# Kernel tuning notes

Hardware: AMD Instinct MI355X
Metric: run time of the kernel (lower is better)

## Reference

```python
import jax, jax.numpy as jnp
import numpy as np

B, N, DIM, H, CH, M = 2, 65536, 256, 8, 32, 64
INNER = H * CH  # 256


def setup_inputs() -> dict:
    key = jax.random.key(0)
    ks = jax.random.split(key, 13)
    s = 0.02
    return {
        "x": jax.random.normal(ks[0], (B, N, DIM), dtype=jnp.float32),
        "W_fx": jax.random.normal(ks[1], (DIM, INNER), dtype=jnp.float32) * s,
        "b_fx": jnp.zeros((INNER,), dtype=jnp.float32),
        "W_x": jax.random.normal(ks[2], (DIM, INNER), dtype=jnp.float32) * s,
        "b_x": jnp.zeros((INNER,), dtype=jnp.float32),
        "W_slice": jax.random.normal(ks[3], (CH, M), dtype=jnp.float32) * s,
        "b_slice": jnp.zeros((M,), dtype=jnp.float32),
        "temperature": 0.5 * jnp.ones((1, H, 1, 1), dtype=jnp.float32),
        "W_q": jax.random.normal(ks[4], (CH, CH), dtype=jnp.float32) * s,
        "W_k": jax.random.normal(ks[5], (CH, CH), dtype=jnp.float32) * s,
        "W_v": jax.random.normal(ks[6], (CH, CH), dtype=jnp.float32) * s,
        "W_out": jax.random.normal(ks[7], (INNER, DIM), dtype=jnp.float32) * s,
        "b_out": jnp.zeros((DIM,), dtype=jnp.float32),
    }


def reference(x, W_fx, b_fx, W_x, b_x, W_slice, b_slice, temperature,
              W_q, W_k, W_v, W_out, b_out):
    b, n, _ = x.shape
    h, ch, m = H, CH, M
    # input projections -> [B, H, N, Ch]
    fx_mid = (x @ W_fx + b_fx).reshape(b, n, h, ch).transpose(0, 2, 1, 3)
    x_mid = (x @ W_x + b_x).reshape(b, n, h, ch).transpose(0, 2, 1, 3)
    # learned soft-slice weights: [B, H, N, M]
    temp = jnp.clip(temperature, 0.1, 5.0)
    logits = (x_mid @ W_slice + b_slice) / temp
    slice_weights = jax.nn.softmax(logits, axis=-1)
    slice_norm = slice_weights.sum(axis=2)  # [B, H, M]
    # aggregate N points into M slice tokens: [B, H, M, Ch]
    slice_token = jnp.einsum('bhnc,bhng->bhgc', fx_mid, slice_weights)
    slice_token = slice_token / (slice_norm + 1e-5)[:, :, :, None]
    # small attention among slice tokens
    q = slice_token @ W_q
    k = slice_token @ W_k
    v = slice_token @ W_v
    scale = ch ** (-0.5)
    attn = jax.nn.softmax(jnp.einsum('bhgc,bhkc->bhgk', q, k) * scale, axis=-1)
    out_slice = attn @ v  # [B, H, M, Ch]
    # scatter back to N points: [B, H, N, Ch] -> [B, N, H*Ch]
    out_x = jnp.einsum('bhgc,bhng->bhnc', out_slice, slice_weights)
    out_x = out_x.transpose(0, 2, 1, 3).reshape(b, n, h * ch)
    return out_x @ W_out + b_out
```

## Files before the change

kernel.cpp:

```cpp
#include <hip/hip_runtime.h>

#define N_ 65536

typedef unsigned int  uint32;
typedef unsigned short ushort;
typedef float  f32x4 __attribute__((ext_vector_type(4)));
typedef short  s16x8 __attribute__((ext_vector_type(8)));
typedef uint32 u32x2 __attribute__((ext_vector_type(2)));
typedef uint32 u32x4 __attribute__((ext_vector_type(4)));

__device__ __forceinline__ uint32 f2bf(float f){
  union{float f; uint32 i;} v; v.f=f;
  return (v.i + 0x7fffu + ((v.i>>16)&1u)) >> 16;
}
__device__ __forceinline__ float bfl(uint32 h){
  union{uint32 i; float f;} v; v.i = h<<16; return v.f;
}
__device__ __forceinline__ uint32 pk2(float a, float b){
  return f2bf(a) | (f2bf(b)<<16);
}
__device__ __forceinline__ f32x4 mfma16(s16x8 a, s16x8 b, f32x4 c){
  return __builtin_amdgcn_mfma_f32_16x16x32_bf16(a,b,c,0,0,0);
}
__device__ __forceinline__ s16x8 mk8(uint32 a, uint32 b, uint32 c, uint32 d){
  union{u32x4 u; s16x8 s;} v; v.u = (u32x4){a,b,c,d}; return v.s;
}

__global__ __launch_bounds__(256) void prep_kernel(
    const float* __restrict__ Wfx, const float* __restrict__ Wx,
    const float* __restrict__ Wsl, const float* __restrict__ bsl,
    const float* __restrict__ bx,  const float* __restrict__ temp,
    ushort* __restrict__ WlT, ushort* __restrict__ WfxT, float* __restrict__ blT)
{
  const int blk = blockIdx.x, t = threadIdx.x;
  if (blk < 512){
    const int m = blk, h = m>>6, mp = m&63;
    const float tmp = fminf(fmaxf(temp[h],0.1f),5.0f);
    float s = 0.f;
    #pragma unroll
    for (int cc=0; cc<32; cc++) s += Wx[t*256 + h*32+cc]*Wsl[cc*64+mp];
    WlT[m*256+t] = (ushort)f2bf(s/tmp);
    if (t==0){
      float bs = bsl[mp];
      for (int cc=0; cc<32; cc++) bs += bx[h*32+cc]*Wsl[cc*64+mp];
      blT[m] = bs/tmp;
    }
  } else {
    const int c = blk-512;
    WfxT[c*256+t] = (ushort)f2bf(Wfx[t*256+c]);
  }
}

__global__ __launch_bounds__(256) void xbf_kernel(const float* __restrict__ x, ushort* __restrict__ xbf)
{
  const size_t i = ((size_t)blockIdx.x*256 + threadIdx.x)*8;
  const float4* xp = (const float4*)(x + i);
  const float4 a = xp[0], b = xp[1];
  u32x4 o; o.x = pk2(a.x,a.y); o.y = pk2(a.z,a.w); o.z = pk2(b.x,b.y); o.w = pk2(b.z,b.w);
  *(u32x4*)(xbf + i) = o;
}

__global__ __launch_bounds__(512)
void k1a_kernel(
    const ushort* __restrict__ xbf,
    const ushort* __restrict__ WlT,
    const ushort* __restrict__ WfxT,
    const float* __restrict__ blT,
    const float* __restrict__ bfx,
    ushort* __restrict__ swg2,
    float* __restrict__ stp,
    float* __restrict__ normp)
{
  __shared__ __align__(16) char smem[98304];
  const int t = threadIdx.x;
  const int w = t>>6, l = t&63, rg = l>>4, c16 = l&15;
  const int blk = blockIdx.x;
  const int tile0 = ((blk&127)<<3) + ((blk>>7)<<10);

  char* swb = smem + 65536 + (w<<12);

  f32x4 pc[2][4];
  #pragma unroll
  for (int i=0;i<2;i++)
    #pragma unroll
    for (int j=0;j<4;j++) pc[i][j] = (f32x4){0.f,0.f,0.f,0.f};
  f32x4 nacc[4];
  #pragma unroll
  for (int i=0;i<4;i++) nacc[i] = (f32x4){0.f,0.f,0.f,0.f};
  float bfv[2];
  #pragma unroll
  for (int cf=0;cf<2;cf++) bfv[cf] = bfx[(w<<5)+(cf<<4)+c16];

  #define STAGE(TILE, BUF) { \
    const int gnS = (int)((TILE)<<6); \
    _Pragma("unroll") \
    for (int p=0;p<4;p++){ \
      const int row = (p<<4) + (t>>5); \
      const int z = (t&31)<<4; \
      const char* g = (const char*)xbf + (((size_t)(gnS+row))<<9) + (size_t)(z ^ ((row&7)<<4)); \
      uint32* ldsp = (uint32*)(smem + ((BUF)<<15) + (p<<13) + ((t>>6)<<10)); \
      __builtin_amdgcn_global_load_lds((const uint32*)g, ldsp, 16, 0, 0); \
    } }

  STAGE(tile0, 0);
  __syncthreads();

  for (int it=0; it<8; ++it){
    const int cur = it&1;
    const int tile = tile0 + it;
    if (it<7) STAGE(tile+1, cur^1);
    const char* Xb = smem + (cur<<15);
    const long gn0 = (long)tile<<6;

    #pragma unroll
    for (int ch=0; ch<2; ch++){
      f32x4 accA[4][2];
      #pragma unroll
      for (int mf=0;mf<4;mf++)
        #pragma unroll
        for (int nfc=0;nfc<2;nfc++) accA[mf][nfc] = (f32x4){0.f,0.f,0.f,0.f};
      #pragma unroll
      for (int kb=0;kb<8;kb++){
        s16x8 aW[4], xv[2];
        #pragma unroll
        for (int mf=0;mf<4;mf++)
          aW[mf] = *(const s16x8*)(WlT + (((w<<6)+(mf<<4)+c16)<<8) + (kb<<5)+(rg<<3));
        #pragma unroll
        for (int nfc=0;nfc<2;nfc++){
          const int row = (ch<<5) + (nfc<<4) + c16;
          xv[nfc] = *(const s16x8*)(Xb + (row<<9) + (((kb<<6)+(rg<<4)) ^ ((row&7)<<4)));
        }
        #pragma unroll
        for (int mf=0;mf<4;mf++)
          #pragma unroll
          for (int nfc=0;nfc<2;nfc++)
            accA[mf][nfc] = mfma16(aW[mf], xv[nfc], accA[mf][nfc]);
      }
      #pragma unroll
      for (int nfc=0;nfc<2;nfc++){
        f32x4 v[4];
        float mx = -3.0e38f;
        #pragma unroll
        for (int mf=0;mf<4;mf++){
          const f32x4 bl4 = *(const f32x4*)(blT + (w<<6)+(mf<<4)+(rg<<2));
          v[mf] = accA[mf][nfc] + bl4;
          mx = fmaxf(mx, fmaxf(fmaxf(v[mf].x, v[mf].y), fmaxf(v[mf].z, v[mf].w)));
        }
        mx = fmaxf(mx, __shfl_xor(mx,16));
        mx = fmaxf(mx, __shfl_xor(mx,32));
        float s = 0.f;
        #pragma unroll
        for (int mf=0;mf<4;mf++){
          v[mf].x = __expf(v[mf].x-mx); v[mf].y = __expf(v[mf].y-mx);
          v[mf].z = __expf(v[mf].z-mx); v[mf].w = __expf(v[mf].w-mx);
          s += v[mf].x+v[mf].y+v[mf].z+v[mf].w;
        }
        s += __shfl_xor(s,16);
        s += __shfl_xor(s,32);
        const float inv = 1.0f/s;
        const int pb = (int)(gn0>>4) + (ch<<1) + nfc;
        #pragma unroll
        for (int mf=0;mf<4;mf++){
          f32x4 sv = v[mf]*inv;
          nacc[mf] += sv;
          u32x2 p; p.x = pk2(sv.x, sv.y); p.y = pk2(sv.z, sv.w);
          *(u32x2*)(swg2 + ((((((size_t)pb<<3)+w)<<2)+mf)<<8) + (rg<<6) + (c16<<2)) = p;
          const uint32 px = (uint32)__shfl_xor((int)p.x, 1);
          const uint32 py = (uint32)__shfl_xor((int)p.y, 1);
          const bool ev = ((c16&1)==0);
          const uint32 s0 = ev ? (uint32)p.x : py;
          const uint32 s1 = ev ? px : (uint32)p.y;
          const uint32 wA = (s0 & 0xffffu) | (s1<<16);
          const uint32 wB = (s0>>16) | (s1 & 0xffff0000u);
          const int rowA = (mf<<4) + (rg<<2) + (ev?0:2);
          const int cbyt = ((nfc<<4) | (c16 & ~1)) << 1;
          *(uint32*)(swb + ((rowA  )<<6) + (cbyt ^ (((rowA  )&7)<<3))) = wA;
          *(uint32*)(swb + ((rowA+1)<<6) + (cbyt ^ (((rowA+1)&7)<<3))) = wB;
        }
      }

      f32x4 accB[2][2];
      #pragma unroll
      for (int pf=0;pf<2;pf++)
        #pragma unroll
        for (int cf=0;cf<2;cf++) accB[pf][cf] = (f32x4){0.f,0.f,0.f,0.f};
      #pragma unroll
      for (int kb=0;kb<8;kb++){
        s16x8 bW[2], xv[2];
        #pragma unroll
        for (int cf=0;cf<2;cf++)
          bW[cf] = *(const s16x8*)(WfxT + (((w<<5)+(cf<<4)+c16)<<8) + (kb<<5)+(rg<<3));
        #pragma unroll
        for (int pf=0;pf<2;pf++){
          const int row = (ch<<5) + (pf<<4) + c16;
          xv[pf] = *(const s16x8*)(Xb + (row<<9) + (((kb<<6)+(rg<<4)) ^ ((row&7)<<4)));
        }
        #pragma unroll
        for (int pf=0;pf<2;pf++)
          #pragma unroll
          for (int cf=0;cf<2;cf++)
            accB[pf][cf] = mfma16(xv[pf], bW[cf], accB[pf][cf]);
      }
      u32x4 afu[2][2];
      #pragma unroll
      for (int cf=0;cf<2;cf++)
        #pragma unroll
        for (int pf=0;pf<2;pf++){
          const float v0 = accB[pf][cf].x+bfv[cf], v1 = accB[pf][cf].y+bfv[cf];
          const float v2 = accB[pf][cf].z+bfv[cf], v3 = accB[pf][cf].w+bfv[cf];
          const uint32 h0=f2bf(v0), h1=f2bf(v1), h2=f2bf(v2), h3=f2bf(v3);
          afu[cf][pf].x = h0|(h1<<16);
          afu[cf][pf].y = h2|(h3<<16);
          afu[cf][pf].z = f2bf(v0-bfl(h0)) | (f2bf(v1-bfl(h1))<<16);
          afu[cf][pf].w = f2bf(v2-bfl(h2)) | (f2bf(v3-bfl(h3))<<16);
        }
      asm volatile("s_waitcnt lgkmcnt(0)" ::: "memory");
      __builtin_amdgcn_sched_barrier(0);

      #pragma unroll
      for (int pf=0;pf<2;pf++)
        #pragma unroll
        for (int mf=0;mf<4;mf++){
          const int row = (mf<<4)+c16;
          const u32x2 q = *(const u32x2*)(swb + (row<<6) + ((((pf<<5)+(rg<<3)) ^ ((row&7)<<3))));
          const s16x8 bdup = mk8(q.x, q.y, q.x, q.y);
          pc[0][mf] = mfma16(mk8(afu[0][pf].x,afu[0][pf].y,afu[0][pf].z,afu[0][pf].w), bdup, pc[0][mf]);
          pc[1][mf] = mfma16(mk8(afu[1][pf].x,afu[1][pf].y,afu[1][pf].z,afu[1][pf].w), bdup, pc[1][mf]);
        }
      asm volatile("s_waitcnt lgkmcnt(0)" ::: "memory");
      __builtin_amdgcn_sched_barrier(0);
    }
    __syncthreads();
  }
  #undef STAGE

  #pragma unroll
  for (int m=0;m<4;m++){
    #pragma unroll
    for (int d=1; d<16; d<<=1){
      nacc[m].x += __shfl_xor(nacc[m].x, d);
      nacc[m].y += __shfl_xor(nacc[m].y, d);
      nacc[m].z += __shfl_xor(nacc[m].z, d);
      nacc[m].w += __shfl_xor(nacc[m].w, d);
    }
  }
  if (c16==0){
    #pragma unroll
    for (int m=0;m<4;m++)
      *(f32x4*)(normp + (((blk<<3)+w)<<6) + (m<<4) + (rg<<2)) = nacc[m];
  }
  const long sb = ((long)((blk<<3)+w))<<11;
  #pragma unroll
  for (int cf=0;cf<2;cf++)
    #pragma unroll
    for (int mf=0;mf<4;mf++)
      #pragma unroll
      for (int r=0;r<4;r++){
        const int cc = (cf<<4)+(rg<<2)+r;
        stp[sb + (cc<<6) + (mf<<4) + c16] = pc[cf][mf][r];
      }
}

__global__ __launch_bounds__(256) void k2a_kernel(float* __restrict__ stp, float* __restrict__ normp)
{
  const int gid = blockIdx.x;
  const int bh = gid>>3, grp = gid&7;
  const int b = bh>>3, h = bh&7;
  const int t = threadIdx.x;
  const int blk0 = (b<<7) + (grp<<4);
  f32x4 a0 = {0,0,0,0}, a1 = {0,0,0,0};
  for (int i=0;i<16;i++){
    const f32x4* p = (const f32x4*)(stp + ((((size_t)(blk0+i)<<3)+h)<<11) + ((size_t)t<<3));
    a0 += p[0]; a1 += p[1];
  }
  f32x4* q = (f32x4*)(stp + ((((size_t)blk0<<3)+h)<<11) + ((size_t)t<<3));
  q[0] = a0; q[1] = a1;
  if (t<8){
    f32x4 n0 = {0,0,0,0}, n1 = {0,0,0,0};
    for (int i=0;i<16;i++){
      const f32x4* p = (const f32x4*)(normp + (((blk0+i)<<3)+h)*64 + (t<<3));
      n0 += p[0]; n1 += p[1];
    }
    f32x4* qn = (f32x4*)(normp + ((blk0<<3)+h)*64 + (t<<3));
    qn[0] = n0; qn[1] = n1;
  }
}

__global__ __launch_bounds__(256) void k2b_kernel(
    const float* __restrict__ stp, const float* __restrict__ normp,
    const float* __restrict__ Wq, const float* __restrict__ Wk, const float* __restrict__ Wv,
    const float* __restrict__ Wout, ushort* __restrict__ OS2Th, ushort* __restrict__ OS2Tl)
{
  __shared__ float nrmL[64];
  __shared__ float tok[2048];
  __shared__ float qL[2048], kL[2048], vL[2048];
  __shared__ float sc[4096];
  __shared__ float osL[2048];
  const int bh = blockIdx.x; const int b = bh>>3, h = bh&7;
  const int t = threadIdx.x;

  if (t<64){
    float s = 0.f;
    for (int g=0; g<8; g++) s += normp[((((b<<7)+(g<<4))<<3)+h)*64 + t];
    nrmL[t] = s;
  }
  __syncthreads();
  {
    f32x4 a0 = {0,0,0,0}, a1 = {0,0,0,0};
    for (int g=0; g<8; g++){
      const f32x4* p = (const f32x4*)(stp + ((((size_t)((b<<7)+(g<<4))<<3)+h)<<11) + ((size_t)t<<3));
      a0 += p[0]; a1 += p[1];
    }
    const int c = t>>3, m0 = (t&7)<<3;
    #pragma unroll
    for (int j=0;j<4;j++) tok[(m0+j)*32 + c]   = a0[j] / (nrmL[m0+j]   + 1e-5f);
    #pragma unroll
    for (int j=0;j<4;j++) tok[(m0+4+j)*32 + c] = a1[j] / (nrmL[m0+4+j] + 1e-5f);
  }
  __syncthreads();

  const int g = t>>2, q4 = t&3;
  float aq[8]={0,0,0,0,0,0,0,0}, ak2[8]={0,0,0,0,0,0,0,0}, av[8]={0,0,0,0,0,0,0,0};
  for (int kk=0; kk<32; kk++){
    const float tv = tok[(g<<5)+kk];
    const int wo = kk*32 + (q4<<3);
    #pragma unroll
    for (int j=0;j<8;j++){
      aq[j]  = fmaf(tv, Wq[wo+j], aq[j]);
      ak2[j] = fmaf(tv, Wk[wo+j], ak2[j]);
      av[j]  = fmaf(tv, Wv[wo+j], av[j]);
    }
  }
  #pragma unroll
  for (int j=0;j<8;j++){
    qL[(g<<5)+(q4<<3)+j]=aq[j];
    kL[(g<<5)+(q4<<3)+j]=ak2[j];
    vL[(g<<5)+(q4<<3)+j]=av[j];
  }
  __syncthreads();

  const float scale = 0.17677669529663689f;
  float svv[16]; float mx = -3.0e38f;
  for (int mm=0;mm<16;mm++){
    const int m = (q4<<4)+mm;
    float s2 = 0.f;
    #pragma unroll
    for (int c=0;c<32;c++) s2 = fmaf(qL[(g<<5)+c], kL[(m<<5)+c], s2);
    s2 *= scale;
    svv[mm] = s2; mx = fmaxf(mx, s2);
  }
  mx = fmaxf(mx, __shfl_xor(mx,1));
  mx = fmaxf(mx, __shfl_xor(mx,2));
  float ssum = 0.f;
  for (int mm=0;mm<16;mm++){ svv[mm] = __expf(svv[mm]-mx); ssum += svv[mm]; }
  ssum += __shfl_xor(ssum,1); ssum += __shfl_xor(ssum,2);
  const float isum = 1.0f/ssum;
  for (int mm=0;mm<16;mm++) sc[(g<<6) + (q4<<4) + mm] = svv[mm]*isum;
  __syncthreads();

  float os[8]={0,0,0,0,0,0,0,0};
  for (int m=0;m<64;m++){
    const float a = sc[(g<<6)+m];
    const int vo = (m<<5)+(q4<<3);
    #pragma unroll
    for (int j=0;j<8;j++) os[j] = fmaf(a, vL[vo+j], os[j]);
  }
  #pragma unroll
  for (int j=0;j<8;j++) osL[(g<<5)+(q4<<3)+j] = os[j];
  __syncthreads();

  const int d = t;
  float wcol[32];
  #pragma unroll
  for (int c=0;c<32;c++) wcol[c] = Wout[(h*32+c)*256 + d];
  uint32* orh = (uint32*)(OS2Th + ((size_t)(b*256+d))*512 + h*64);
  uint32* orl = (uint32*)(OS2Tl + ((size_t)(b*256+d))*512 + h*64);
  #pragma unroll 4
  for (int g2=0; g2<32; g2++){
    float s0=0.f, s1=0.f;
    #pragma unroll
    for (int c=0;c<32;c++){
      s0 = fmaf(osL[((g2*2  )<<5)+c], wcol[c], s0);
      s1 = fmaf(osL[((g2*2+1)<<5)+c], wcol[c], s1);
    }
    const uint32 h0 = f2bf(s0), h1 = f2bf(s1);
    orh[g2] = h0 | (h1<<16);
    orl[g2] = f2bf(s0 - bfl(h0)) | (f2bf(s1 - bfl(h1)) << 16);
  }
}

__global__ __launch_bounds__(256) void k3_kernel(
    const ushort* __restrict__ swg2,
    const ushort* __restrict__ OS2Th,
    const ushort* __restrict__ OS2Tl,
    const float* __restrict__ bout,
    float* __restrict__ out)
{
  const int t = threadIdx.x, w = t>>6, l = t&63, rg = l>>4, c16 = l&15;
  const int blk = blockIdx.x;
  const long gn0 = (long)blk<<6;
  const int b = blk>>10;
  f32x4 acc[4][4];
  #pragma unroll
  for (int r=0;r<4;r++)
    #pragma unroll
    for (int c=0;c<4;c++) acc[r][c] = (f32x4){0.f,0.f,0.f,0.f};
  const long obb = (((long)(b<<8) + (w<<6))<<9);
  for (int kb=0;kb<16;kb++){
    const int h3 = kb>>1;
    const int mb = ((kb&1)<<1) + (rg>>1);
    const int pkt = (rg&1)<<1;
    s16x8 aS[4];
    #pragma unroll
    for (int r=0;r<4;r++){
      const long pb = (gn0>>4) + r;
      const ushort* bp = swg2 + ((((pb<<3)+h3)<<2) + mb)*256 + (c16<<2);
      const u32x2 lo = *(const u32x2*)(bp + (pkt<<6));
      const u32x2 hi = *(const u32x2*)(bp + ((pkt+1)<<6));
      aS[r] = mk8(lo.x, lo.y, hi.x, hi.y);
    }
    #pragma unroll
    for (int c=0;c<4;c++){
      const long ro = obb + ((long)((c<<4)+c16)<<9) + (kb<<5)+(rg<<3);
      const s16x8 bhv = *(const s16x8*)(OS2Th + ro);
      const s16x8 blv = *(const s16x8*)(OS2Tl + ro);
      #pragma unroll
      for (int r=0;r<4;r++)
        acc[r][c] = mfma16(aS[r], bhv, acc[r][c]);
      #pragma unroll
      for (int r=0;r<4;r++)
        acc[r][c] = mfma16(aS[r], blv, acc[r][c]);
    }
  }
  float bo[4];
  #pragma unroll
  for (int c=0;c<4;c++) bo[c] = bout[(w<<6)+(c<<4)+c16];
  #pragma unroll
  for (int r=0;r<4;r++)
    #pragma unroll
    for (int c=0;c<4;c++)
      #pragma unroll
      for (int rr=0;rr<4;rr++)
        out[((gn0 + (r<<4)+(rg<<2)+rr)<<8) + (w<<6)+(c<<4)+c16] = acc[r][c][rr] + bo[c];
}

extern "C" void kernel_launch(void* const* d_in, const int* in_sizes, int n_in,
                              void* d_out, int out_size, void* d_ws, size_t ws_size,
                              hipStream_t stream)
{
  const float* x     = (const float*)d_in[0];
  const float* Wfx   = (const float*)d_in[1];
  const float* bfx   = (const float*)d_in[2];
  const float* Wx    = (const float*)d_in[3];
  const float* bx    = (const float*)d_in[4];
  const float* Wsl   = (const float*)d_in[5];
  const float* bsl   = (const float*)d_in[6];
  const float* temp  = (const float*)d_in[7];
  const float* Wq    = (const float*)d_in[8];
  const float* Wk    = (const float*)d_in[9];
  const float* Wv    = (const float*)d_in[10];
  const float* Wout  = (const float*)d_in[11];
  const float* bout  = (const float*)d_in[12];
  float* out = (float*)d_out;

  char* ws = (char*)d_ws;
  ushort* WlT   = (ushort*)(ws);
  ushort* WfxT  = (ushort*)(ws + 262144);
  float*  blT   = (float*) (ws + 393216);
  ushort* swg2  = (ushort*)(ws + 395264);
  float*  stp   = (float*) (ws + 134612992);
  float*  normp = (float*) (ws + 151390208);
  ushort* OS2Th = (ushort*)(ws + 151914496);
  ushort* OS2Tl = (ushort*)(ws + 152438784);

  ushort* xbf = (ushort*)d_out;

  prep_kernel<<<dim3(768), dim3(256), 0, stream>>>(Wfx, Wx, Wsl, bsl, bx, temp, WlT, WfxT, blT);
  xbf_kernel<<<dim3(16384), dim3(256), 0, stream>>>(x, xbf);
  k1a_kernel<<<dim3(256), dim3(512), 0, stream>>>(xbf, WlT, WfxT, blT, bfx, swg2, stp, normp);
  k2a_kernel<<<dim3(128), dim3(256), 0, stream>>>(stp, normp);
  k2b_kernel<<<dim3(16), dim3(256), 0, stream>>>(stp, normp, Wq, Wk, Wv, Wout, OS2Th, OS2Tl);
  k3_kernel<<<dim3(2048), dim3(256), 0, stream>>>(swg2, OS2Th, OS2Tl, bout, out);
}
```

Measured before the change: 519.7 us.

## Recompute slice weights in output kernel instead of storing them to global memory

The first pass no longer writes the bf16 slice-weight tensor (about 134 MB) to global memory. The output kernel now reloads the bf16 input rows, recomputes the logits GEMM and softmax per head, and feeds the result from shared memory into the output projection. The first kernel also drops its double-buffered staging for a single buffer, processes 4 tiles per block over twice as many blocks, and the reduction kernels are adjusted to match. This trades a large global write and read for a second slice-logit GEMM plus softmax, and it loses the overlap between loading and compute in the first kernel.

Result: slower. 760.7 us (+46.4%).

```diff
diff --git a/kernel.cpp b/kernel.cpp
--- a/kernel.cpp
+++ b/kernel.cpp
@@ -61,23 +61,22 @@
 }
 
 __global__ __launch_bounds__(512)
-void k1a_kernel(
+void k1b_kernel(
     const ushort* __restrict__ xbf,
     const ushort* __restrict__ WlT,
     const ushort* __restrict__ WfxT,
     const float* __restrict__ blT,
     const float* __restrict__ bfx,
-    ushort* __restrict__ swg2,
     float* __restrict__ stp,
     float* __restrict__ normp)
 {
-  __shared__ __align__(16) char smem[98304];
+  __shared__ __align__(16) char smem[65536];
   const int t = threadIdx.x;
   const int w = t>>6, l = t&63, rg = l>>4, c16 = l&15;
   const int blk = blockIdx.x;
-  const int tile0 = ((blk&127)<<3) + ((blk>>7)<<10);
-
-  char* swb = smem + 65536 + (w<<12);
+  const int tile0 = ((blk&255)<<2) + ((blk>>8)<<10);
+
+  char* swb = smem + 32768 + (w<<12);
 
   f32x4 pc[2][4];
   #pragma unroll
@@ -91,26 +90,23 @@
   #pragma unroll
   for (int cf=0;cf<2;cf++) bfv[cf] = bfx[(w<<5)+(cf<<4)+c16];
 
-  #define STAGE(TILE, BUF) { \
+  #define STAGE(TILE) { \
     const int gnS = (int)((TILE)<<6); \
     _Pragma("unroll") \
     for (int p=0;p<4;p++){ \
       const int row = (p<<4) + (t>>5); \
       const int z = (t&31)<<4; \
       const char* g = (const char*)xbf + (((size_t)(gnS+row))<<9) + (size_t)(z ^ ((row&7)<<4)); \
-      uint32* ldsp = (uint32*)(smem + ((BUF)<<15) + (p<<13) + ((t>>6)<<10)); \
+      uint32* ldsp = (uint32*)(smem + (p<<13) + ((t>>6)<<10)); \
       __builtin_amdgcn_global_load_lds((const uint32*)g, ldsp, 16, 0, 0); \
     } }
 
-  STAGE(tile0, 0);
-  __syncthreads();
-
-  for (int it=0; it<8; ++it){
-    const int cur = it&1;
-    const int tile = tile0 + it;
-    if (it<7) STAGE(tile+1, cur^1);
-    const char* Xb = smem + (cur<<15);
-    const long gn0 = (long)tile<<6;
+  STAGE(tile0);
+  __syncthreads();
+
+  for (int it=0; it<4; ++it){
+    const long gn0 = (long)(tile0+it)<<6;
+    (void)gn0;
 
     #pragma unroll
     for (int ch=0; ch<2; ch++){
@@ -128,7 +124,7 @@
         #pragma unroll
         for (int nfc=0;nfc<2;nfc++){
           const int row = (ch<<5) + (nfc<<4) + c16;
-          xv[nfc] = *(const s16x8*)(Xb + (row<<9) + (((kb<<6)+(rg<<4)) ^ ((row&7)<<4)));
+          xv[nfc] = *(const s16x8*)(smem + (row<<9) + (((kb<<6)+(rg<<4)) ^ ((row&7)<<4)));
         }
         #pragma unroll
         for (int mf=0;mf<4;mf++)
@@ -158,13 +154,11 @@
         s += __shfl_xor(s,16);
         s += __shfl_xor(s,32);
         const float inv = 1.0f/s;
-        const int pb = (int)(gn0>>4) + (ch<<1) + nfc;
         #pragma unroll
         for (int mf=0;mf<4;mf++){
           f32x4 sv = v[mf]*inv;
           nacc[mf] += sv;
           u32x2 p; p.x = pk2(sv.x, sv.y); p.y = pk2(sv.z, sv.w);
-          *(u32x2*)(swg2 + ((((((size_t)pb<<3)+w)<<2)+mf)<<8) + (rg<<6) + (c16<<2)) = p;
           const uint32 px = (uint32)__shfl_xor((int)p.x, 1);
           const uint32 py = (uint32)__shfl_xor((int)p.y, 1);
           const bool ev = ((c16&1)==0);
@@ -193,7 +187,7 @@
         #pragma unroll
         for (int pf=0;pf<2;pf++){
           const int row = (ch<<5) + (pf<<4) + c16;
-          xv[pf] = *(const s16x8*)(Xb + (row<<9) + (((kb<<6)+(rg<<4)) ^ ((row&7)<<4)));
+          xv[pf] = *(const s16x8*)(smem + (row<<9) + (((kb<<6)+(rg<<4)) ^ ((row&7)<<4)));
         }
         #pragma unroll
         for (int pf=0;pf<2;pf++)
@@ -231,6 +225,7 @@
       __builtin_amdgcn_sched_barrier(0);
     }
     __syncthreads();
+    if (it<3){ STAGE(tile0+it+1); __syncthreads(); }
   }
   #undef STAGE
 
@@ -267,9 +262,9 @@
   const int bh = gid>>3, grp = gid&7;
   const int b = bh>>3, h = bh&7;
   const int t = threadIdx.x;
-  const int blk0 = (b<<7) + (grp<<4);
+  const int blk0 = (b<<8) + (grp<<5);
   f32x4 a0 = {0,0,0,0}, a1 = {0,0,0,0};
-  for (int i=0;i<16;i++){
+  for (int i=0;i<32;i++){
     const f32x4* p = (const f32x4*)(stp + ((((size_t)(blk0+i)<<3)+h)<<11) + ((size_t)t<<3));
     a0 += p[0]; a1 += p[1];
   }
@@ -277,7 +272,7 @@
   q[0] = a0; q[1] = a1;
   if (t<8){
     f32x4 n0 = {0,0,0,0}, n1 = {0,0,0,0};
-    for (int i=0;i<16;i++){
+    for (int i=0;i<32;i++){
       const f32x4* p = (const f32x4*)(normp + (((blk0+i)<<3)+h)*64 + (t<<3));
       n0 += p[0]; n1 += p[1];
     }
@@ -301,14 +296,14 @@
 
   if (t<64){
     float s = 0.f;
-    for (int g=0; g<8; g++) s += normp[((((b<<7)+(g<<4))<<3)+h)*64 + t];
+    for (int g=0; g<8; g++) s += normp[((((b<<8)+(g<<5))<<3)+h)*64 + t];
     nrmL[t] = s;
   }
   __syncthreads();
   {
     f32x4 a0 = {0,0,0,0}, a1 = {0,0,0,0};
     for (int g=0; g<8; g++){
-      const f32x4* p = (const f32x4*)(stp + ((((size_t)((b<<7)+(g<<4))<<3)+h)<<11) + ((size_t)t<<3));
+      const f32x4* p = (const f32x4*)(stp + ((((size_t)((b<<8)+(g<<5))<<3)+h)<<11) + ((size_t)t<<3));
       a0 += p[0]; a1 += p[1];
     }
     const int c = t>>3, m0 = (t&7)<<3;
@@ -389,59 +384,120 @@
   }
 }
 
-__global__ __launch_bounds__(256) void k3_kernel(
-    const ushort* __restrict__ swg2,
+__global__ __launch_bounds__(256)
+void k3_kernel(
+    const ushort* __restrict__ xbf,
+    const ushort* __restrict__ WlT,
+    const float* __restrict__ blT,
     const ushort* __restrict__ OS2Th,
     const ushort* __restrict__ OS2Tl,
     const float* __restrict__ bout,
     float* __restrict__ out)
 {
-  const int t = threadIdx.x, w = t>>6, l = t&63, rg = l>>4, c16 = l&15;
+  __shared__ __align__(16) char smem[40960];
+  const int t = threadIdx.x;
+  const int w = t>>6, l = t&63, rg = l>>4, c16 = l&15;
   const int blk = blockIdx.x;
   const long gn0 = (long)blk<<6;
   const int b = blk>>10;
+
+  #pragma unroll
+  for (int p=0;p<8;p++){
+    const int row = (p<<3) + (t>>5);
+    const int z = (t&31)<<4;
+    const char* g = (const char*)xbf + (((size_t)(gn0+row))<<9) + (size_t)(z ^ ((row&7)<<4));
+    uint32* ldsp = (uint32*)(smem + (p<<12) + ((t>>6)<<10));
+    __builtin_amdgcn_global_load_lds((const uint32*)g, ldsp, 16, 0, 0);
+  }
+  __syncthreads();
+
   f32x4 acc[4][4];
   #pragma unroll
-  for (int r=0;r<4;r++)
-    #pragma unroll
-    for (int c=0;c<4;c++) acc[r][c] = (f32x4){0.f,0.f,0.f,0.f};
-  const long obb = (((long)(b<<8) + (w<<6))<<9);
-  for (int kb=0;kb<16;kb++){
-    const int h3 = kb>>1;
-    const int mb = ((kb&1)<<1) + (rg>>1);
-    const int pkt = (rg&1)<<1;
-    s16x8 aS[4];
-    #pragma unroll
-    for (int r=0;r<4;r++){
-      const long pb = (gn0>>4) + r;
-      const ushort* bp = swg2 + ((((pb<<3)+h3)<<2) + mb)*256 + (c16<<2);
-      const u32x2 lo = *(const u32x2*)(bp + (pkt<<6));
-      const u32x2 hi = *(const u32x2*)(bp + ((pkt+1)<<6));
-      aS[r] = mk8(lo.x, lo.y, hi.x, hi.y);
-    }
-    #pragma unroll
-    for (int c=0;c<4;c++){
-      const long ro = obb + ((long)((c<<4)+c16)<<9) + (kb<<5)+(rg<<3);
-      const s16x8 bhv = *(const s16x8*)(OS2Th + ro);
-      const s16x8 blv = *(const s16x8*)(OS2Tl + ro);
-      #pragma unroll
-      for (int r=0;r<4;r++)
-        acc[r][c] = mfma16(aS[r], bhv, acc[r][c]);
-      #pragma unroll
-      for (int r=0;r<4;r++)
-        acc[r][c] = mfma16(aS[r], blv, acc[r][c]);
-    }
-  }
-  float bo[4];
-  #pragma unroll
-  for (int c=0;c<4;c++) bo[c] = bout[(w<<6)+(c<<4)+c16];
-  #pragma unroll
-  for (int r=0;r<4;r++)
-    #pragma unroll
-    for (int c=0;c<4;c++)
-      #pragma unroll
-      for (int rr=0;rr<4;rr++)
-        out[((gn0 + (r<<4)+(rg<<2)+rr)<<8) + (w<<6)+(c<<4)+c16] = acc[r][c][rr] + bo[c];
+  for (int i=0;i<4;i++)
+    #pragma unroll
+    for (int j=0;j<4;j++) acc[i][j] = (f32x4){0.f,0.f,0.f,0.f};
+
+  const int xrow = (w<<4) + c16;
+
+  for (int h=0; h<8; ++h){
+    f32x4 accA[4];
+    #pragma unroll
+    for (int mf=0;mf<4;mf++) accA[mf] = (f32x4){0.f,0.f,0.f,0.f};
+    #pragma unroll
+    for (int kb=0;kb<8;kb++){
+      s16x8 aW[4];
+      #pragma unroll
+      for (int mf=0;mf<4;mf++)
+        aW[mf] = *(const s16x8*)(WlT + (((h<<6)+(mf<<4)+c16)<<8) + (kb<<5)+(rg<<3));
+      const s16x8 xv = *(const s16x8*)(smem + (xrow<<9) + (((kb<<6)+(rg<<4)) ^ ((c16&7)<<4)));
+      #pragma unroll
+      for (int mf=0;mf<4;mf++)
+        accA[mf] = mfma16(aW[mf], xv, accA[mf]);
+    }
+    {
+      f32x4 v[4];
+      float mx = -3.0e38f;
+      #pragma unroll
+      for (int mf=0;mf<4;mf++){
+        const f32x4 bl4 = *(const f32x4*)(blT + (h<<6)+(mf<<4)+(rg<<2));
+        v[mf] = accA[mf] + bl4;
+        mx = fmaxf(mx, fmaxf(fmaxf(v[mf].x, v[mf].y), fmaxf(v[mf].z, v[mf].w)));
+      }
+      mx = fmaxf(mx, __shfl_xor(mx,16));
+      mx = fmaxf(mx, __shfl_xor(mx,32));
+      float s = 0.f;
+      #pragma unroll
+      for (int mf=0;mf<4;mf++){
+        v[mf].x = __expf(v[mf].x-mx); v[mf].y = __expf(v[mf].y-mx);
+        v[mf].z = __expf(v[mf].z-mx); v[mf].w = __expf(v[mf].w-mx);
+        s += v[mf].x+v[mf].y+v[mf].z+v[mf].w;
+      }
+      s += __shfl_xor(s,16);
+      s += __shfl_xor(s,32);
+      const float inv = 1.0f/s;
+      #pragma unroll
+      for (int mf=0;mf<4;mf++){
+        f32x4 sv = v[mf]*inv;
+        u32x2 p; p.x = pk2(sv.x, sv.y); p.y = pk2(sv.z, sv.w);
+        *(u32x2*)(smem + 32768 + (xrow<<7) + (((mf<<5)+(rg<<3)) ^ ((c16&7)<<4))) = p;
+      }
+    }
+    __syncthreads();
+
+    #pragma unroll
+    for (int kb2=0;kb2<2;kb2++){
+      s16x8 bfr[4];
+      #pragma unroll
+      for (int pf=0;pf<4;pf++){
+        const int prow = (pf<<4)+c16;
+        bfr[pf] = *(const s16x8*)(smem + 32768 + (prow<<7) + (((kb2<<6)+(rg<<4)) ^ ((c16&7)<<4)));
+      }
+      #pragma unroll
+      for (int df=0;df<4;df++){
+        const long ro = (((long)(b<<8) + (w<<6)+(df<<4)+c16)<<9) + (h<<6) + (kb2<<5)+(rg<<3);
+        const s16x8 aOh = *(const s16x8*)(OS2Th + ro);
+        const s16x8 aOl = *(const s16x8*)(OS2Tl + ro);
+        #pragma unroll
+        for (int pf=0;pf<4;pf++)
+          acc[df][pf] = mfma16(aOh, bfr[pf], acc[df][pf]);
+        #pragma unroll
+        for (int pf=0;pf<4;pf++)
+          acc[df][pf] = mfma16(aOl, bfr[pf], acc[df][pf]);
+      }
+    }
+    __syncthreads();
+  }
+
+  #pragma unroll
+  for (int df=0;df<4;df++){
+    const int d0 = (w<<6)+(df<<4)+(rg<<2);
+    const f32x4 bo = *(const f32x4*)(bout + d0);
+    #pragma unroll
+    for (int pf=0;pf<4;pf++){
+      float* o = out + ((gn0 + (pf<<4)+c16)<<8) + d0;
+      *(f32x4*)o = acc[df][pf] + bo;
+    }
+  }
 }
 
 extern "C" void kernel_launch(void* const* d_in, const int* in_sizes, int n_in,
@@ -467,18 +523,16 @@
   ushort* WlT   = (ushort*)(ws);
   ushort* WfxT  = (ushort*)(ws + 262144);
   float*  blT   = (float*) (ws + 393216);
-  ushort* swg2  = (ushort*)(ws + 395264);
-  float*  stp   = (float*) (ws + 134612992);
-  float*  normp = (float*) (ws + 151390208);
-  ushort* OS2Th = (ushort*)(ws + 151914496);
-  ushort* OS2Tl = (ushort*)(ws + 152438784);
-
-  ushort* xbf = (ushort*)d_out;
+  ushort* xbf   = (ushort*)(ws + 395264);
+  float*  stp   = (float*) (ws + 67504128);
+  float*  normp = (float*) (ws + 101058560);
+  ushort* OS2Th = (ushort*)(ws + 102107136);
+  ushort* OS2Tl = (ushort*)(ws + 102631424);
 
   prep_kernel<<<dim3(768), dim3(256), 0, stream>>>(Wfx, Wx, Wsl, bsl, bx, temp, WlT, WfxT, blT);
   xbf_kernel<<<dim3(16384), dim3(256), 0, stream>>>(x, xbf);
-  k1a_kernel<<<dim3(256), dim3(512), 0, stream>>>(xbf, WlT, WfxT, blT, bfx, swg2, stp, normp);
+  k1b_kernel<<<dim3(512), dim3(512), 0, stream>>>(xbf, WlT, WfxT, blT, bfx, stp, normp);
   k2a_kernel<<<dim3(128), dim3(256), 0, stream>>>(stp, normp);
   k2b_kernel<<<dim3(16), dim3(256), 0, stream>>>(stp, normp, Wq, Wk, Wv, Wout, OS2Th, OS2Tl);
-  k3_kernel<<<dim3(2048), dim3(256), 0, stream>>>(swg2, OS2Th, OS2Tl, bout, out);
-}
+  k3_kernel<<<dim3(2048), dim3(256), 0, stream>>>(xbf, WlT, blT, OS2Th, OS2Tl, bout, out);
+}
```

## Fuse fp32-to-bf16 conversion of x into k1a and double its grid

Applied to the files above, without the earlier changes.

Removes the separate xbf conversion kernel: k1a now loads fp32 x directly, converts it to bf16 and writes it swizzled into LDS, dropping the async double-buffered global_load_lds pipeline in favour of synchronous single-buffer staging. LDS per block drops to 64KB with launch_bounds(512,4), and the grid doubles to 512 blocks of 4 tiles each. The partial-sum buffers and the k2a/k2b reductions are reindexed for the new block count, and the stp partials are moved into the output buffer. This saves a full write and re-read of bf16 x but loses load/compute overlap inside k1a, relying on higher occupancy to hide global latency.

Measured after the change: 709.7 us. 1.37x slower.

```diff
diff --git a/kernel.cpp b/kernel.cpp
--- a/kernel.cpp
+++ b/kernel.cpp
@@ -51,18 +51,9 @@
   }
 }
 
-__global__ __launch_bounds__(256) void xbf_kernel(const float* __restrict__ x, ushort* __restrict__ xbf)
-{
-  const size_t i = ((size_t)blockIdx.x*256 + threadIdx.x)*8;
-  const float4* xp = (const float4*)(x + i);
-  const float4 a = xp[0], b = xp[1];
-  u32x4 o; o.x = pk2(a.x,a.y); o.y = pk2(a.z,a.w); o.z = pk2(b.x,b.y); o.w = pk2(b.z,b.w);
-  *(u32x4*)(xbf + i) = o;
-}
-
-__global__ __launch_bounds__(512)
+__global__ __launch_bounds__(512, 4)
 void k1a_kernel(
-    const ushort* __restrict__ xbf,
+    const float* __restrict__ x,
     const ushort* __restrict__ WlT,
     const ushort* __restrict__ WfxT,
     const float* __restrict__ blT,
@@ -71,13 +62,13 @@
     float* __restrict__ stp,
     float* __restrict__ normp)
 {
-  __shared__ __align__(16) char smem[98304];
+  __shared__ __align__(16) char smem[65536];
   const int t = threadIdx.x;
   const int w = t>>6, l = t&63, rg = l>>4, c16 = l&15;
   const int blk = blockIdx.x;
-  const int tile0 = ((blk&127)<<3) + ((blk>>7)<<10);
-
-  char* swb = smem + 65536 + (w<<12);
+  const int tile0 = ((blk&255)<<2) + ((blk>>8)<<10);
+
+  char* swb = smem + 32768 + (w<<12);
 
   f32x4 pc[2][4];
   #pragma unroll
@@ -91,26 +82,23 @@
   #pragma unroll
   for (int cf=0;cf<2;cf++) bfv[cf] = bfx[(w<<5)+(cf<<4)+c16];
 
-  #define STAGE(TILE, BUF) { \
-    const int gnS = (int)((TILE)<<6); \
-    _Pragma("unroll") \
-    for (int p=0;p<4;p++){ \
-      const int row = (p<<4) + (t>>5); \
-      const int z = (t&31)<<4; \
-      const char* g = (const char*)xbf + (((size_t)(gnS+row))<<9) + (size_t)(z ^ ((row&7)<<4)); \
-      uint32* ldsp = (uint32*)(smem + ((BUF)<<15) + (p<<13) + ((t>>6)<<10)); \
-      __builtin_amdgcn_global_load_lds((const uint32*)g, ldsp, 16, 0, 0); \
-    } }
-
-  STAGE(tile0, 0);
-  __syncthreads();
-
-  for (int it=0; it<8; ++it){
-    const int cur = it&1;
+  for (int it=0; it<4; ++it){
     const int tile = tile0 + it;
-    if (it<7) STAGE(tile+1, cur^1);
-    const char* Xb = smem + (cur<<15);
     const long gn0 = (long)tile<<6;
+
+    __syncthreads();
+    {
+      const float4* xs = (const float4*)(x + (gn0<<8));
+      #pragma unroll
+      for (int p=0;p<8;p++){
+        const int f = t + (p<<9);
+        const int row = f>>6, q = f&63;
+        const float4 v = xs[f];
+        u32x2 uu; uu.x = pk2(v.x, v.y); uu.y = pk2(v.z, v.w);
+        *(u32x2*)(smem + (row<<9) + ((q<<3) ^ ((row&7)<<4))) = uu;
+      }
+    }
+    __syncthreads();
 
     #pragma unroll
     for (int ch=0; ch<2; ch++){
@@ -128,7 +116,7 @@
         #pragma unroll
         for (int nfc=0;nfc<2;nfc++){
           const int row = (ch<<5) + (nfc<<4) + c16;
-          xv[nfc] = *(const s16x8*)(Xb + (row<<9) + (((kb<<6)+(rg<<4)) ^ ((row&7)<<4)));
+          xv[nfc] = *(const s16x8*)(smem + (row<<9) + (((kb<<6)+(rg<<4)) ^ ((row&7)<<4)));
         }
         #pragma unroll
         for (int mf=0;mf<4;mf++)
@@ -193,7 +181,7 @@
         #pragma unroll
         for (int pf=0;pf<2;pf++){
           const int row = (ch<<5) + (pf<<4) + c16;
-          xv[pf] = *(const s16x8*)(Xb + (row<<9) + (((kb<<6)+(rg<<4)) ^ ((row&7)<<4)));
+          xv[pf] = *(const s16x8*)(smem + (row<<9) + (((kb<<6)+(rg<<4)) ^ ((row&7)<<4)));
         }
         #pragma unroll
         for (int pf=0;pf<2;pf++)
@@ -230,9 +218,7 @@
       asm volatile("s_waitcnt lgkmcnt(0)" ::: "memory");
       __builtin_amdgcn_sched_barrier(0);
     }
-    __syncthreads();
-  }
-  #undef STAGE
+  }
 
   #pragma unroll
   for (int m=0;m<4;m++){
@@ -267,9 +253,9 @@
   const int bh = gid>>3, grp = gid&7;
   const int b = bh>>3, h = bh&7;
   const int t = threadIdx.x;
-  const int blk0 = (b<<7) + (grp<<4);
+  const int blk0 = (b<<8) + (grp<<5);
   f32x4 a0 = {0,0,0,0}, a1 = {0,0,0,0};
-  for (int i=0;i<16;i++){
+  for (int i=0;i<32;i++){
     const f32x4* p = (const f32x4*)(stp + ((((size_t)(blk0+i)<<3)+h)<<11) + ((size_t)t<<3));
     a0 += p[0]; a1 += p[1];
   }
@@ -277,7 +263,7 @@
   q[0] = a0; q[1] = a1;
   if (t<8){
     f32x4 n0 = {0,0,0,0}, n1 = {0,0,0,0};
-    for (int i=0;i<16;i++){
+    for (int i=0;i<32;i++){
       const f32x4* p = (const f32x4*)(normp + (((blk0+i)<<3)+h)*64 + (t<<3));
       n0 += p[0]; n1 += p[1];
     }
@@ -301,14 +287,14 @@
 
   if (t<64){
     float s = 0.f;
-    for (int g=0; g<8; g++) s += normp[((((b<<7)+(g<<4))<<3)+h)*64 + t];
+    for (int g=0; g<8; g++) s += normp[((((b<<8)+(g<<5))<<3)+h)*64 + t];
     nrmL[t] = s;
   }
   __syncthreads();
   {
     f32x4 a0 = {0,0,0,0}, a1 = {0,0,0,0};
     for (int g=0; g<8; g++){
-      const f32x4* p = (const f32x4*)(stp + ((((size_t)((b<<7)+(g<<4))<<3)+h)<<11) + ((size_t)t<<3));
+      const f32x4* p = (const f32x4*)(stp + ((((size_t)((b<<8)+(g<<5))<<3)+h)<<11) + ((size_t)t<<3));
       a0 += p[0]; a1 += p[1];
     }
     const int c = t>>3, m0 = (t&7)<<3;
@@ -468,16 +454,14 @@
   ushort* WfxT  = (ushort*)(ws + 262144);
   float*  blT   = (float*) (ws + 393216);
   ushort* swg2  = (ushort*)(ws + 395264);
-  float*  stp   = (float*) (ws + 134612992);
-  float*  normp = (float*) (ws + 151390208);
-  ushort* OS2Th = (ushort*)(ws + 151914496);
-  ushort* OS2Tl = (ushort*)(ws + 152438784);
-
-  ushort* xbf = (ushort*)d_out;
+  float*  normp = (float*) (ws + 134612992);
+  ushort* OS2Th = (ushort*)(ws + 135661568);
+  ushort* OS2Tl = (ushort*)(ws + 136185856);
+
+  float* stp = (float*)d_out;
 
   prep_kernel<<<dim3(768), dim3(256), 0, stream>>>(Wfx, Wx, Wsl, bsl, bx, temp, WlT, WfxT, blT);
-  xbf_kernel<<<dim3(16384), dim3(256), 0, stream>>>(x, xbf);
-  k1a_kernel<<<dim3(256), dim3(512), 0, stream>>>(xbf, WlT, WfxT, blT, bfx, swg2, stp, normp);
+  k1a_kernel<<<dim3(512), dim3(512), 0, stream>>>(x, WlT, WfxT, blT, bfx, swg2, stp, normp);
   k2a_kernel<<<dim3(128), dim3(256), 0, stream>>>(stp, normp);
   k2b_kernel<<<dim3(16), dim3(256), 0, stream>>>(stp, normp, Wq, Wk, Wv, Wout, OS2Th, OS2Tl);
   k3_kernel<<<dim3(2048), dim3(256), 0, stream>>>(swg2, OS2Th, OS2Tl, bout, out);
```
